# Optimization experiments

Hardware: AMD Instinct MI355X
Metric: run time of the kernel (lower is better)

The kernel has to match this reference:

```python
import jax, jax.numpy as jnp
import numpy as np

N0 = 1373      # hardcoded node-type split in the original forward
TAO = 0.4
EPS = 1e-12


def _l2norm(x, axis):
    # matches torch F.normalize(p=2): x / max(||x||, eps)
    n = jnp.sqrt(jnp.sum(x * x, axis=axis, keepdims=True))
    return x / jnp.maximum(n, EPS)


def setup_inputs() -> dict:
    key = jax.random.key(0)
    ks = jax.random.split(key, 12)
    N, E, D_IN, F, H, D = 20000, 320000, 256, 32, 8, 32
    feat = jax.random.normal(ks[0], (N, D_IN), jnp.float32)
    sloc = jax.random.normal(ks[1], (N, D), jnp.float32)
    topo_fea = jax.random.normal(ks[2], (N, D), jnp.float32)
    src = jax.random.randint(ks[3], (E,), 0, N)
    dst = jax.random.randint(ks[4], (E,), 0, N)
    e_feat = jax.random.randint(ks[5], (E,), 0, 4)
    s = 1.0 / np.sqrt(D_IN)
    W_proj0 = jax.random.normal(ks[6], (D_IN, H * F), jnp.float32) * s
    W_proj1 = jax.random.normal(ks[7], (D_IN, H * F), jnp.float32) * s
    W_prob = jax.random.normal(ks[8], (H, F, F), jnp.float32) * (1.0 / np.sqrt(F))
    W_res0 = jax.random.normal(ks[9], (D_IN, H * F), jnp.float32) * s
    W_res1 = jax.random.normal(ks[10], (D_IN, H * F), jnp.float32) * s
    etype_attn = jnp.ones((4,), jnp.float32)
    return dict(feat=feat, sloc=sloc, topo_fea=topo_fea, src=src, dst=dst,
                e_feat=e_feat, W_proj0=W_proj0, W_proj1=W_proj1, W_prob=W_prob,
                W_res0=W_res0, W_res1=W_res1, etype_attn=etype_attn)


def reference(feat, sloc, topo_fea, src, dst, e_feat,
              W_proj0, W_proj1, W_prob, W_res0, W_res1, etype_attn):
    N = feat.shape[0]
    H, F = W_prob.shape[0], W_prob.shape[2]
    sloc3 = sloc[:, None, :]        # (N,1,D) -- .unsqueeze(1)
    topo3 = topo_fea[:, None, :]

    # per-type node projection
    feat_src = jnp.concatenate(
        [feat[:N0] @ W_proj0, feat[N0:] @ W_proj1], axis=0).reshape(N, H, F)
    # per-head attention feature: softmax(tanh(fc4prob_i(.)), dim=feat)
    ft_attn = jax.nn.softmax(
        jnp.tanh(jnp.einsum('nhf,hfg->nhg', feat_src, W_prob)), axis=2)
    # F.normalize over the NODE dimension (dim=0), as in original
    ft_norm = _l2norm(feat_src, axis=0)

    sloc_n = _l2norm(sloc3, axis=2)
    topo_n = _l2norm(topo3, axis=2)

    # edge attention scores
    a = jnp.sum(ft_attn[dst] * ft_norm[src], axis=2, keepdims=True)   # (E,H,1)
    cos_s = jnp.sum(sloc_n[src] * sloc_n[dst], axis=2, keepdims=True)  # (E,1,1)
    cos_t = jnp.sum(topo_n[src] * topo_n[dst], axis=2, keepdims=True)
    sim = (TAO * cos_s + (1.0 - TAO) * cos_t + 1.0) / 2.0             # (E,1,1)
    e = (sim * a * etype_attn[e_feat][:, None, None])[:, :, 0]        # (E,H)

    # edge softmax: segment softmax over incoming edges of each dst node
    m = jax.ops.segment_max(e, dst, num_segments=N)                   # (N,H)
    ex = jnp.exp(e - m[dst])
    z = jax.ops.segment_sum(ex, dst, num_segments=N)
    att = ex / z[dst]                                                 # (E,H)

    # three u_mul_e + sum aggregations
    aw = att[:, :, None]                                              # (E,H,1)
    rst = jax.ops.segment_sum(feat_src[src] * aw, dst, num_segments=N)  # (N,H,F)
    sl2 = jax.ops.segment_sum(sloc3[src] * aw, dst, num_segments=N)     # (N,H,D)
    tp2 = jax.ops.segment_sum(topo3[src] * aw, dst, num_segments=N)     # (N,H,D)

    resval = jnp.concatenate(
        [feat[:N0] @ W_res0, feat[N0:] @ W_res1], axis=0).reshape(N, H, F)
    out_fea = jax.nn.relu(rst + resval).mean(axis=1)   # (N,F)
    out_sloc = (sl2 + sloc3).mean(axis=1)              # (N,D)
    out_topo = (tp2 + topo3).mean(axis=1)              # (N,D)
    return out_fea, out_sloc, out_topo
```

## Files before the change

kernel.cpp:

```cpp
#include <hip/hip_runtime.h>
#include <math.h>

#define HN0 1373
#define BM 128
#define BN 128
#define BK 32
#define LDT 40

typedef __attribute__((ext_vector_type(8))) short short8;
typedef __attribute__((ext_vector_type(4))) float f32x4;

__device__ inline unsigned short f2bf(float f) {
  unsigned int u = __float_as_uint(f);
  unsigned int r = (u + 0x7FFFu + ((u >> 16) & 1u)) >> 16;
  return (unsigned short)r;
}
__device__ inline float bflo(unsigned int u) { return __uint_as_float(u << 16); }
__device__ inline float bfhi(unsigned int u) { return __uint_as_float(u & 0xFFFF0000u); }

__device__ inline uint4 pack8bf(float4 a, float4 b) {
  uint4 o;
  o.x = (unsigned)f2bf(a.x) | ((unsigned)f2bf(a.y) << 16);
  o.y = (unsigned)f2bf(a.z) | ((unsigned)f2bf(a.w) << 16);
  o.z = (unsigned)f2bf(b.x) | ((unsigned)f2bf(b.y) << 16);
  o.w = (unsigned)f2bf(b.z) | ((unsigned)f2bf(b.w) << 16);
  return o;
}

__global__ __launch_bounds__(256) void prep(
    const float* __restrict__ Wp0, const float* __restrict__ Wr0,
    const float* __restrict__ Wp1, const float* __restrict__ Wr1,
    unsigned short* __restrict__ BTw,
    const float* __restrict__ sloc, const float* __restrict__ topo,
    float* __restrict__ inv_s, float* __restrict__ inv_t,
    unsigned short* __restrict__ slt,
    const int* __restrict__ dst, int* __restrict__ deg, int N, int E) {
  int b = blockIdx.x;
  int tid = threadIdx.x;
  int nodeBlocks = (N + 7) / 8;
  if (b < 1024) {
    int n = b & 511, g = b >> 9;
    const float* W;
    if (g == 0) W = (n < 256) ? Wp0 : Wr0;
    else        W = (n < 256) ? Wp1 : Wr1;
    int c = n & 255;
    BTw[(size_t)g * 512 * 256 + (size_t)n * 256 + tid] = f2bf(W[(size_t)tid * 256 + c]);
  } else if (b < 1024 + nodeBlocks) {
    int node = (b - 1024) * 8 + (tid >> 5);
    int d = tid & 31;
    if (node >= N) return;
    float s = sloc[(size_t)node * 32 + d];
    float t = topo[(size_t)node * 32 + d];
    float ss = s * s, tt = t * t;
#pragma unroll
    for (int m = 16; m >= 1; m >>= 1) {
      ss += __shfl_xor(ss, m);
      tt += __shfl_xor(tt, m);
    }
    if (d == 0) {
      inv_s[node] = 1.f / fmaxf(sqrtf(ss), 1e-12f);
      inv_t[node] = 1.f / fmaxf(sqrtf(tt), 1e-12f);
    }
    slt[(size_t)node * 64 + d] = f2bf(s);
    slt[(size_t)node * 64 + 32 + d] = f2bf(t);
  } else {
    int e = (b - 1024 - nodeBlocks) * 256 + tid;
    if (e < E) atomicAdd(&deg[dst[e]], 1);
  }
}

__global__ __launch_bounds__(256) void gemm_mfma(
    const float* __restrict__ A, const unsigned short* __restrict__ BTw,
    unsigned short* __restrict__ feat_bf, float* __restrict__ resval, int N) {
  __shared__ __align__(16) unsigned short As[BM * LDT];
  __shared__ __align__(16) unsigned short Bs[BN * LDT];
  int tid = threadIdx.x;
  int lane = tid & 63;
  int w = tid >> 6;
  int wr = w >> 1, wc = w & 1;

  int g0t = (HN0 + BM - 1) / BM;
  int bx = blockIdx.x;
  bool g1 = bx >= g0t;
  int rowBase = g1 ? HN0 + (bx - g0t) * BM : bx * BM;
  int rowEnd = g1 ? N : HN0;
  const unsigned short* BT = BTw + (g1 ? (size_t)512 * 256 : 0);
  int colBase = blockIdx.y * BN;

  int r0 = tid >> 2;
  int kp = (tid & 3) << 3;
  int ar1 = min(rowBase + r0, rowEnd - 1);
  int ar2 = min(rowBase + r0 + 64, rowEnd - 1);
  const float* aP1 = A + (size_t)ar1 * 256 + kp;
  const float* aP2 = A + (size_t)ar2 * 256 + kp;
  const unsigned short* bP1 = BT + (size_t)(colBase + r0) * 256 + kp;
  const unsigned short* bP2 = bP1 + (size_t)64 * 256;
  int wo1 = r0 * LDT + kp;
  int wo2 = (r0 + 64) * LDT + kp;

  int q = lane >> 4;
  int fr = lane & 15;
  int aOff = (wr * 64 + fr) * LDT + q * 8;
  int bOff = (wc * 64 + fr) * LDT + q * 8;

  f32x4 acc[4][4] = {};

  float4 fa1a = *reinterpret_cast<const float4*>(aP1);
  float4 fa1b = *reinterpret_cast<const float4*>(aP1 + 4);
  float4 fa2a = *reinterpret_cast<const float4*>(aP2);
  float4 fa2b = *reinterpret_cast<const float4*>(aP2 + 4);
  uint4 rb1 = *reinterpret_cast<const uint4*>(bP1);
  uint4 rb2 = *reinterpret_cast<const uint4*>(bP2);

  for (int t = 0; t < 8; ++t) {
    *reinterpret_cast<uint4*>(&As[wo1]) = pack8bf(fa1a, fa1b);
    *reinterpret_cast<uint4*>(&As[wo2]) = pack8bf(fa2a, fa2b);
    *reinterpret_cast<uint4*>(&Bs[wo1]) = rb1;
    *reinterpret_cast<uint4*>(&Bs[wo2]) = rb2;
    __syncthreads();
    if (t < 7) {
      int ko = (t + 1) * BK;
      fa1a = *reinterpret_cast<const float4*>(aP1 + ko);
      fa1b = *reinterpret_cast<const float4*>(aP1 + ko + 4);
      fa2a = *reinterpret_cast<const float4*>(aP2 + ko);
      fa2b = *reinterpret_cast<const float4*>(aP2 + ko + 4);
      rb1 = *reinterpret_cast<const uint4*>(bP1 + ko);
      rb2 = *reinterpret_cast<const uint4*>(bP2 + ko);
    }
    short8 af[4], bf4[4];
#pragma unroll
    for (int i = 0; i < 4; ++i) {
      af[i] = *reinterpret_cast<const short8*>(&As[aOff + i * 16 * LDT]);
      bf4[i] = *reinterpret_cast<const short8*>(&Bs[bOff + i * 16 * LDT]);
    }
#pragma unroll
    for (int i = 0; i < 4; ++i)
#pragma unroll
      for (int j = 0; j < 4; ++j)
        acc[i][j] = __builtin_amdgcn_mfma_f32_16x16x32_bf16(af[i], bf4[j], acc[i][j], 0, 0, 0);
    __syncthreads();
  }

  if (colBase < 256) {
#pragma unroll
    for (int i = 0; i < 4; ++i) {
      int rb = rowBase + wr * 64 + i * 16 + q * 4;
#pragma unroll
      for (int j = 0; j < 4; ++j) {
        int col = colBase + wc * 64 + j * 16 + fr;
        f32x4 v = acc[i][j];
#pragma unroll
        for (int rr = 0; rr < 4; ++rr) {
          int r = rb + rr;
          if (r < rowEnd) feat_bf[(size_t)r * 256 + col] = f2bf(v[rr]);
        }
      }
    }
  } else {
    int cOff = colBase - 256;
#pragma unroll
    for (int i = 0; i < 4; ++i) {
      int rb = rowBase + wr * 64 + i * 16 + q * 4;
#pragma unroll
      for (int j = 0; j < 4; ++j) {
        int col = cOff + wc * 64 + j * 16 + fr;
        f32x4 v = acc[i][j];
#pragma unroll
        for (int rr = 0; rr < 4; ++rr) {
          int r = rb + rr;
          if (r < rowEnd) resval[(size_t)r * 256 + col] = v[rr];
        }
      }
    }
  }
}

__global__ __launch_bounds__(256) void attn_probs(
    const unsigned short* __restrict__ feat_bf, const float* __restrict__ W_prob,
    unsigned short* __restrict__ ft_attn, float* __restrict__ col_ss, int N) {
  __shared__ float WL[8192];
  __shared__ float fsL[16 * 256];
  int tid = threadIdx.x;
  for (int i = tid; i < 8192; i += 256) WL[i] = W_prob[i];
  int nodeBase = blockIdx.x * 16;
  float ssp = 0.f;
  for (int i = 0; i < 16; ++i) {
    int n = nodeBase + i;
    float v = (n < N) ? __uint_as_float((unsigned)feat_bf[(size_t)n * 256 + tid] << 16) : 0.f;
    fsL[i * 256 + tid] = v;
    ssp += v * v;
  }
  atomicAdd(&col_ss[tid], ssp);
  __syncthreads();
  int h = tid >> 5, g = tid & 31;
  for (int i = 0; i < 16; ++i) {
    int n = nodeBase + i;
    if (n >= N) break;
    float t = 0.f;
    const float* wp = &WL[h * 1024 + g];
    const float* fr = &fsL[i * 256 + h * 32];
#pragma unroll
    for (int f = 0; f < 32; ++f) t = fmaf(fr[f], wp[f * 32], t);
    t = tanhf(t);
    float mx = t;
#pragma unroll
    for (int s = 16; s >= 1; s >>= 1) mx = fmaxf(mx, __shfl_xor(mx, s));
    float ex = __expf(t - mx);
    float sm = ex;
#pragma unroll
    for (int s = 16; s >= 1; s >>= 1) sm += __shfl_xor(sm, s);
    ft_attn[(size_t)n * 256 + tid] = f2bf(ex / sm);
  }
}

__global__ __launch_bounds__(512) void scan_block(const int* __restrict__ deg,
                                                  int* __restrict__ start,
                                                  int* __restrict__ bsum, int n) {
  __shared__ int buf[512];
  int tid = threadIdx.x;
  int gid = blockIdx.x * 512 + tid;
  int v = (gid < n) ? deg[gid] : 0;
  buf[tid] = v;
  __syncthreads();
  for (int off = 1; off < 512; off <<= 1) {
    int t = (tid >= off) ? buf[tid - off] : 0;
    __syncthreads();
    buf[tid] += t;
    __syncthreads();
  }
  if (gid < n) start[gid] = buf[tid] - v;
  if (tid == 511) bsum[blockIdx.x] = buf[511];
}

__global__ __launch_bounds__(256) void mid_small(float* __restrict__ col_ss,
                                                 int* __restrict__ bsum, int nb) {
  int tid = threadIdx.x;
  col_ss[tid] = 1.f / fmaxf(sqrtf(col_ss[tid]), 1e-12f);
  __shared__ int buf[128];
  if (tid < nb) buf[tid] = bsum[tid];
  __syncthreads();
  if (tid == 0) {
    int run = 0;
    for (int i = 0; i < nb; ++i) { int v = buf[i]; buf[i] = run; run += v; }
  }
  __syncthreads();
  if (tid < nb) bsum[tid] = buf[tid];
}

__global__ __launch_bounds__(256) void fill_sim(
    const int* __restrict__ src, const int* __restrict__ dst,
    const int* __restrict__ e_feat, const float* __restrict__ etype_attn,
    const unsigned short* __restrict__ slt,
    const float* __restrict__ inv_s, const float* __restrict__ inv_t,
    const int* __restrict__ start, const int* __restrict__ bsum,
    int* __restrict__ cursor, int* __restrict__ csr_src,
    float* __restrict__ csr_w, int E) {
  int tid = threadIdx.x;
  int j = tid & 7;
  int e = blockIdx.x * 32 + (tid >> 3);
  if (e >= E) return;
  int s = src[e], d = dst[e];
  const unsigned short* ps = slt + (size_t)s * 64 + j * 4;
  const unsigned short* pd = slt + (size_t)d * 64 + j * 4;
  uint2 sa = *reinterpret_cast<const uint2*>(ps);
  uint2 sb = *reinterpret_cast<const uint2*>(pd);
  uint2 ta = *reinterpret_cast<const uint2*>(ps + 32);
  uint2 tb = *reinterpret_cast<const uint2*>(pd + 32);
  float cs = bflo(sa.x) * bflo(sb.x) + bfhi(sa.x) * bfhi(sb.x) +
             bflo(sa.y) * bflo(sb.y) + bfhi(sa.y) * bfhi(sb.y);
  float ct = bflo(ta.x) * bflo(tb.x) + bfhi(ta.x) * bfhi(tb.x) +
             bflo(ta.y) * bflo(tb.y) + bfhi(ta.y) * bfhi(tb.y);
#pragma unroll
  for (int m = 4; m >= 1; m >>= 1) {
    cs += __shfl_xor(cs, m);
    ct += __shfl_xor(ct, m);
  }
  if (j == 0) {
    cs *= inv_s[s] * inv_s[d];
    ct *= inv_t[s] * inv_t[d];
    float sim = (0.4f * cs + 0.6f * ct + 1.f) * 0.5f;
    float wv = sim * etype_attn[e_feat[e]];
    int pos = start[d] + bsum[d >> 9] + atomicAdd(&cursor[d], 1);
    csr_src[pos] = s;
    csr_w[pos] = wv;
  }
}

#define GATHER(S, FP, SL, TP)                                                  \
  {                                                                            \
    FP = *reinterpret_cast<const uint2*>(feat_bf + (size_t)(S) * 256 + fb);    \
    const unsigned short* sp_ = slt + (size_t)(S) * 64 + db;                   \
    SL = *reinterpret_cast<const uint2*>(sp_);                                 \
    TP = *reinterpret_cast<const uint2*>(sp_ + 32);                            \
  }

#define CONSUME(FP, SL, TP, WV)                                                \
  {                                                                            \
    float fs0 = bflo(FP.x), fs1 = bfhi(FP.x);                                  \
    float fs2 = bflo(FP.y), fs3 = bfhi(FP.y);                                  \
    float pa = ai4.x * fs0 + ai4.y * fs1 + ai4.z * fs2 + ai4.w * fs3;          \
    pa += __shfl_xor(pa, 1);                                                   \
    pa += __shfl_xor(pa, 2);                                                   \
    pa += __shfl_xor(pa, 4);                                                   \
    float p = __expf(pa * WV);                                                 \
    l += p;                                                                    \
    accf.x = fmaf(p, fs0, accf.x); accf.y = fmaf(p, fs1, accf.y);              \
    accf.z = fmaf(p, fs2, accf.z); accf.w = fmaf(p, fs3, accf.w);              \
    accs.x = fmaf(p, bflo(SL.x), accs.x); accs.y = fmaf(p, bfhi(SL.x), accs.y);\
    accs.z = fmaf(p, bflo(SL.y), accs.z); accs.w = fmaf(p, bfhi(SL.y), accs.w);\
    acct.x = fmaf(p, bflo(TP.x), acct.x); acct.y = fmaf(p, bfhi(TP.x), acct.y);\
    acct.z = fmaf(p, bflo(TP.y), acct.z); acct.w = fmaf(p, bfhi(TP.y), acct.w);\
  }

__global__ __launch_bounds__(256) void edge_aggregate(
    const unsigned short* __restrict__ feat_bf, const float* __restrict__ resval,
    const unsigned short* __restrict__ ft_attn, const float* __restrict__ inv_cn,
    const unsigned short* __restrict__ slt,
    const float* __restrict__ sloc, const float* __restrict__ topo,
    const int* __restrict__ start, const int* __restrict__ bsum,
    const int* __restrict__ deg,
    const int* __restrict__ csr_src, const float* __restrict__ csr_w,
    float* __restrict__ out, int N) {
  int wave = threadIdx.x >> 6;
  int n = blockIdx.x * 4 + wave;
  if (n >= N) return;
  int lane = threadIdx.x & 63;
  int j = lane & 7;
  int fb = (lane >> 3) * 32 + j * 4;
  int db = j * 4;

  uint2 at2 = *reinterpret_cast<const uint2*>(ft_attn + (size_t)n * 256 + fb);
  float4 icn4 = *reinterpret_cast<const float4*>(inv_cn + fb);
  float4 ai4 = make_float4(bflo(at2.x) * icn4.x, bfhi(at2.x) * icn4.y,
                           bflo(at2.y) * icn4.z, bfhi(at2.y) * icn4.w);
  float l = 0.f;
  float4 accf = make_float4(0.f, 0.f, 0.f, 0.f);
  float4 accs = make_float4(0.f, 0.f, 0.f, 0.f);
  float4 acct = make_float4(0.f, 0.f, 0.f, 0.f);
  int s0 = start[n] + bsum[n >> 9];
  int dg = deg[n];

  int sA = 0, sB = 0;
  float wA = 0.f, wB = 0.f;
  uint2 fpA, slA, tpA, fpB, slB, tpB;
  fpA = fpB = slA = slB = tpA = tpB = make_uint2(0u, 0u);
  if (dg > 0) {
    sA = csr_src[s0]; wA = csr_w[s0];
    GATHER(sA, fpA, slA, tpA);
  }
  if (dg > 1) {
    sB = csr_src[s0 + 1]; wB = csr_w[s0 + 1];
    GATHER(sB, fpB, slB, tpB);
  }
  int i = 0;
  for (; i + 1 < dg; i += 2) {
    CONSUME(fpA, slA, tpA, wA);
    if (i + 2 < dg) {
      sA = csr_src[s0 + i + 2]; wA = csr_w[s0 + i + 2];
      GATHER(sA, fpA, slA, tpA);
    }
    CONSUME(fpB, slB, tpB, wB);
    if (i + 3 < dg) {
      sB = csr_src[s0 + i + 3]; wB = csr_w[s0 + i + 3];
      GATHER(sB, fpB, slB, tpB);
    }
  }
  if (i < dg) CONSUME(fpA, slA, tpA, wA);

  float invl = (l > 0.f) ? 1.f / l : 0.f;

  float4 res4 = *reinterpret_cast<const float4*>(resval + (size_t)n * 256 + fb);
  float4 of = make_float4(fmaxf(fmaf(accf.x, invl, res4.x), 0.f),
                          fmaxf(fmaf(accf.y, invl, res4.y), 0.f),
                          fmaxf(fmaf(accf.z, invl, res4.z), 0.f),
                          fmaxf(fmaf(accf.w, invl, res4.w), 0.f));
  float4 os = make_float4(accs.x * invl, accs.y * invl, accs.z * invl, accs.w * invl);
  float4 ot = make_float4(acct.x * invl, acct.y * invl, acct.z * invl, acct.w * invl);
#pragma unroll
  for (int msk = 8; msk <= 32; msk <<= 1) {
    of.x += __shfl_xor(of.x, msk); of.y += __shfl_xor(of.y, msk);
    of.z += __shfl_xor(of.z, msk); of.w += __shfl_xor(of.w, msk);
    os.x += __shfl_xor(os.x, msk); os.y += __shfl_xor(os.y, msk);
    os.z += __shfl_xor(os.z, msk); os.w += __shfl_xor(os.w, msk);
    ot.x += __shfl_xor(ot.x, msk); ot.y += __shfl_xor(ot.y, msk);
    ot.z += __shfl_xor(ot.z, msk); ot.w += __shfl_xor(ot.w, msk);
  }
  if (lane < 8) {
    float4 sln = *reinterpret_cast<const float4*>(sloc + (size_t)n * 32 + db);
    float4 tpn = *reinterpret_cast<const float4*>(topo + (size_t)n * 32 + db);
    float4 o0 = make_float4(of.x * 0.125f, of.y * 0.125f, of.z * 0.125f, of.w * 0.125f);
    float4 o1 = make_float4(fmaf(os.x, 0.125f, sln.x), fmaf(os.y, 0.125f, sln.y),
                            fmaf(os.z, 0.125f, sln.z), fmaf(os.w, 0.125f, sln.w));
    float4 o2 = make_float4(fmaf(ot.x, 0.125f, tpn.x), fmaf(ot.y, 0.125f, tpn.y),
                            fmaf(ot.z, 0.125f, tpn.z), fmaf(ot.w, 0.125f, tpn.w));
    *reinterpret_cast<float4*>(out + (size_t)n * 32 + db) = o0;
    *reinterpret_cast<float4*>(out + (size_t)N * 32 + (size_t)n * 32 + db) = o1;
    *reinterpret_cast<float4*>(out + (size_t)2 * N * 32 + (size_t)n * 32 + db) = o2;
  }
}

extern "C" void kernel_launch(void* const* d_in, const int* in_sizes, int n_in,
                              void* d_out, int out_size, void* d_ws, size_t ws_size,
                              hipStream_t stream) {
  const float* feat = (const float*)d_in[0];
  const float* sloc = (const float*)d_in[1];
  const float* topo = (const float*)d_in[2];
  const int* src = (const int*)d_in[3];
  const int* dst = (const int*)d_in[4];
  const int* e_feat = (const int*)d_in[5];
  const float* W_proj0 = (const float*)d_in[6];
  const float* W_proj1 = (const float*)d_in[7];
  const float* W_prob = (const float*)d_in[8];
  const float* W_res0 = (const float*)d_in[9];
  const float* W_res1 = (const float*)d_in[10];
  const float* etype_attn = (const float*)d_in[11];
  int E = in_sizes[3];
  int N = in_sizes[1] / 32;
  float* out = (float*)d_out;

  char* ws = (char*)d_ws;
  size_t off = 0;
  auto alloc = [&](size_t bytes) -> char* {
    char* p = ws + off;
    off += (bytes + 255) & ~(size_t)255;
    return p;
  };
  int* deg = (int*)alloc((size_t)N * 4);
  int* cursor = (int*)alloc((size_t)N * 4);
  float* col_ss = (float*)alloc(256 * 4);
  size_t zeroBytes = ((char*)col_ss + 256 * 4) - (char*)deg;
  int* startArr = (int*)alloc(((size_t)N + 1) * 4);
  int* bsum = (int*)alloc(128 * 4);
  float* inv_s = (float*)alloc((size_t)N * 4);
  float* inv_t = (float*)alloc((size_t)N * 4);
  int* csr_src = (int*)alloc((size_t)E * 4);
  float* csr_w = (float*)alloc((size_t)E * 4);
  unsigned short* feat_bf = (unsigned short*)alloc((size_t)N * 256 * 2);
  unsigned short* slt = (unsigned short*)alloc((size_t)N * 64 * 2);
  float* resval = (float*)alloc((size_t)N * 256 * 4);
  unsigned short* ft_attn = (unsigned short*)alloc((size_t)N * 256 * 2);
  unsigned short* BTw = (unsigned short*)alloc((size_t)2 * 512 * 256 * 2);

  hipMemsetAsync(deg, 0, zeroBytes, stream);

  int nodeBlocks = (N + 7) / 8;
  int degBlocks = (E + 255) / 256;
  prep<<<1024 + nodeBlocks + degBlocks, 256, 0, stream>>>(
      W_proj0, W_res0, W_proj1, W_res1, BTw, sloc, topo, inv_s, inv_t, slt,
      dst, deg, N, E);

  int g0t = (HN0 + BM - 1) / BM;
  int g1t = (N - HN0 + BM - 1) / BM;
  gemm_mfma<<<dim3(g0t + g1t, 4), 256, 0, stream>>>(feat, BTw, feat_bf, resval, N);

  attn_probs<<<(N + 15) / 16, 256, 0, stream>>>(feat_bf, W_prob, ft_attn, col_ss, N);

  int nb = (N + 511) / 512;
  scan_block<<<nb, 512, 0, stream>>>(deg, startArr, bsum, N);
  mid_small<<<1, 256, 0, stream>>>(col_ss, bsum, nb);

  fill_sim<<<(E + 31) / 32, 256, 0, stream>>>(src, dst, e_feat, etype_attn, slt,
                                              inv_s, inv_t, startArr, bsum,
                                              cursor, csr_src, csr_w, E);

  edge_aggregate<<<(N + 3) / 4, 256, 0, stream>>>(feat_bf, resval, ft_attn, col_ss,
                                                  slt, sloc, topo, startArr, bsum, deg,
                                                  csr_src, csr_w, out, N);
}
```

Baseline: 191.0 us.

## Store resval in bf16, pack CSR as int2, deepen gather pipeline, shrink blocks

The residual GEMM output is now stored as bf16 instead of fp32, which halves its write and read traffic. The CSR source index and weight are interleaved into a single int2 array so each edge needs one load. The edge_aggregate prefetch is raised from two to three edges in flight, and the kernel runs 128-thread blocks with two nodes per block instead of four. The bf16 residual adds rounding error to the feature output.

```diff
diff --git a/kernel.cpp b/kernel.cpp
--- a/kernel.cpp
+++ b/kernel.cpp
@@ -71,7 +71,8 @@
 
 __global__ __launch_bounds__(256) void gemm_mfma(
     const float* __restrict__ A, const unsigned short* __restrict__ BTw,
-    unsigned short* __restrict__ feat_bf, float* __restrict__ resval, int N) {
+    unsigned short* __restrict__ feat_bf, unsigned short* __restrict__ resval,
+    int N) {
   __shared__ __align__(16) unsigned short As[BM * LDT];
   __shared__ __align__(16) unsigned short Bs[BN * LDT];
   int tid = threadIdx.x;
@@ -141,35 +142,19 @@
     __syncthreads();
   }
 
-  if (colBase < 256) {
-#pragma unroll
-    for (int i = 0; i < 4; ++i) {
-      int rb = rowBase + wr * 64 + i * 16 + q * 4;
-#pragma unroll
-      for (int j = 0; j < 4; ++j) {
-        int col = colBase + wc * 64 + j * 16 + fr;
-        f32x4 v = acc[i][j];
-#pragma unroll
-        for (int rr = 0; rr < 4; ++rr) {
-          int r = rb + rr;
-          if (r < rowEnd) feat_bf[(size_t)r * 256 + col] = f2bf(v[rr]);
-        }
-      }
-    }
-  } else {
-    int cOff = colBase - 256;
-#pragma unroll
-    for (int i = 0; i < 4; ++i) {
-      int rb = rowBase + wr * 64 + i * 16 + q * 4;
-#pragma unroll
-      for (int j = 0; j < 4; ++j) {
-        int col = cOff + wc * 64 + j * 16 + fr;
-        f32x4 v = acc[i][j];
-#pragma unroll
-        for (int rr = 0; rr < 4; ++rr) {
-          int r = rb + rr;
-          if (r < rowEnd) resval[(size_t)r * 256 + col] = v[rr];
-        }
+  unsigned short* outp = (colBase < 256) ? feat_bf : resval;
+  int cOff = colBase & 255;
+#pragma unroll
+  for (int i = 0; i < 4; ++i) {
+    int rb = rowBase + wr * 64 + i * 16 + q * 4;
+#pragma unroll
+    for (int j = 0; j < 4; ++j) {
+      int col = cOff + wc * 64 + j * 16 + fr;
+      f32x4 v = acc[i][j];
+#pragma unroll
+      for (int rr = 0; rr < 4; ++rr) {
+        int r = rb + rr;
+        if (r < rowEnd) outp[(size_t)r * 256 + col] = f2bf(v[rr]);
       }
     }
   }
@@ -253,8 +238,7 @@
     const unsigned short* __restrict__ slt,
     const float* __restrict__ inv_s, const float* __restrict__ inv_t,
     const int* __restrict__ start, const int* __restrict__ bsum,
-    int* __restrict__ cursor, int* __restrict__ csr_src,
-    float* __restrict__ csr_w, int E) {
+    int* __restrict__ cursor, int2* __restrict__ csr, int E) {
   int tid = threadIdx.x;
   int j = tid & 7;
   int e = blockIdx.x * 32 + (tid >> 3);
@@ -281,28 +265,34 @@
     float sim = (0.4f * cs + 0.6f * ct + 1.f) * 0.5f;
     float wv = sim * etype_attn[e_feat[e]];
     int pos = start[d] + bsum[d >> 9] + atomicAdd(&cursor[d], 1);
-    csr_src[pos] = s;
-    csr_w[pos] = wv;
-  }
-}
-
-#define GATHER(S, FP, SL, TP)                                                  \
-  {                                                                            \
-    FP = *reinterpret_cast<const uint2*>(feat_bf + (size_t)(S) * 256 + fb);    \
-    const unsigned short* sp_ = slt + (size_t)(S) * 64 + db;                   \
+    csr[pos] = make_int2(s, __float_as_int(wv));
+  }
+}
+
+#define LOADIDX(K, V, W)                                                       \
+  do {                                                                         \
+    int2 c_ = csr[s0 + (K)];                                                   \
+    V = c_.x;                                                                  \
+    W = __int_as_float(c_.y);                                                  \
+  } while (0)
+
+#define GATHER(V, FP, SL, TP)                                                  \
+  do {                                                                         \
+    FP = *reinterpret_cast<const uint2*>(feat_bf + (size_t)(V) * 256 + fb);    \
+    const unsigned short* sp_ = slt + (size_t)(V) * 64 + db;                   \
     SL = *reinterpret_cast<const uint2*>(sp_);                                 \
     TP = *reinterpret_cast<const uint2*>(sp_ + 32);                            \
-  }
-
-#define CONSUME(FP, SL, TP, WV)                                                \
-  {                                                                            \
+  } while (0)
+
+#define CONSUME(W, FP, SL, TP)                                                 \
+  do {                                                                         \
     float fs0 = bflo(FP.x), fs1 = bfhi(FP.x);                                  \
     float fs2 = bflo(FP.y), fs3 = bfhi(FP.y);                                  \
     float pa = ai4.x * fs0 + ai4.y * fs1 + ai4.z * fs2 + ai4.w * fs3;          \
     pa += __shfl_xor(pa, 1);                                                   \
     pa += __shfl_xor(pa, 2);                                                   \
     pa += __shfl_xor(pa, 4);                                                   \
-    float p = __expf(pa * WV);                                                 \
+    float p = __expf(pa * (W));                                                \
     l += p;                                                                    \
     accf.x = fmaf(p, fs0, accf.x); accf.y = fmaf(p, fs1, accf.y);              \
     accf.z = fmaf(p, fs2, accf.z); accf.w = fmaf(p, fs3, accf.w);              \
@@ -310,19 +300,18 @@
     accs.z = fmaf(p, bflo(SL.y), accs.z); accs.w = fmaf(p, bfhi(SL.y), accs.w);\
     acct.x = fmaf(p, bflo(TP.x), acct.x); acct.y = fmaf(p, bfhi(TP.x), acct.y);\
     acct.z = fmaf(p, bflo(TP.y), acct.z); acct.w = fmaf(p, bfhi(TP.y), acct.w);\
-  }
-
-__global__ __launch_bounds__(256) void edge_aggregate(
-    const unsigned short* __restrict__ feat_bf, const float* __restrict__ resval,
+  } while (0)
+
+__global__ __launch_bounds__(128) void edge_aggregate(
+    const unsigned short* __restrict__ feat_bf, const unsigned short* __restrict__ resval,
     const unsigned short* __restrict__ ft_attn, const float* __restrict__ inv_cn,
     const unsigned short* __restrict__ slt,
     const float* __restrict__ sloc, const float* __restrict__ topo,
     const int* __restrict__ start, const int* __restrict__ bsum,
-    const int* __restrict__ deg,
-    const int* __restrict__ csr_src, const float* __restrict__ csr_w,
+    const int* __restrict__ deg, const int2* __restrict__ csr,
     float* __restrict__ out, int N) {
   int wave = threadIdx.x >> 6;
-  int n = blockIdx.x * 4 + wave;
+  int n = blockIdx.x * 2 + wave;
   if (n >= N) return;
   int lane = threadIdx.x & 63;
   int j = lane & 7;
@@ -340,40 +329,33 @@
   int s0 = start[n] + bsum[n >> 9];
   int dg = deg[n];
 
-  int sA = 0, sB = 0;
-  float wA = 0.f, wB = 0.f;
-  uint2 fpA, slA, tpA, fpB, slB, tpB;
-  fpA = fpB = slA = slB = tpA = tpB = make_uint2(0u, 0u);
-  if (dg > 0) {
-    sA = csr_src[s0]; wA = csr_w[s0];
-    GATHER(sA, fpA, slA, tpA);
-  }
-  if (dg > 1) {
-    sB = csr_src[s0 + 1]; wB = csr_w[s0 + 1];
-    GATHER(sB, fpB, slB, tpB);
-  }
+  int vA = 0, vB = 0, vC = 0;
+  float wA = 0.f, wB = 0.f, wC = 0.f;
+  uint2 fpA = make_uint2(0u, 0u), fpB = make_uint2(0u, 0u), fpC = make_uint2(0u, 0u);
+  uint2 slA = make_uint2(0u, 0u), slB = make_uint2(0u, 0u), slC = make_uint2(0u, 0u);
+  uint2 tpA = make_uint2(0u, 0u), tpB = make_uint2(0u, 0u), tpC = make_uint2(0u, 0u);
+  if (dg > 0) { LOADIDX(0, vA, wA); GATHER(vA, fpA, slA, tpA); }
+  if (dg > 1) { LOADIDX(1, vB, wB); GATHER(vB, fpB, slB, tpB); }
+  if (dg > 2) { LOADIDX(2, vC, wC); GATHER(vC, fpC, slC, tpC); }
   int i = 0;
-  for (; i + 1 < dg; i += 2) {
-    CONSUME(fpA, slA, tpA, wA);
-    if (i + 2 < dg) {
-      sA = csr_src[s0 + i + 2]; wA = csr_w[s0 + i + 2];
-      GATHER(sA, fpA, slA, tpA);
-    }
-    CONSUME(fpB, slB, tpB, wB);
-    if (i + 3 < dg) {
-      sB = csr_src[s0 + i + 3]; wB = csr_w[s0 + i + 3];
-      GATHER(sB, fpB, slB, tpB);
-    }
-  }
-  if (i < dg) CONSUME(fpA, slA, tpA, wA);
+  for (; i + 2 < dg; i += 3) {
+    CONSUME(wA, fpA, slA, tpA);
+    if (i + 3 < dg) { LOADIDX(i + 3, vA, wA); GATHER(vA, fpA, slA, tpA); }
+    CONSUME(wB, fpB, slB, tpB);
+    if (i + 4 < dg) { LOADIDX(i + 4, vB, wB); GATHER(vB, fpB, slB, tpB); }
+    CONSUME(wC, fpC, slC, tpC);
+    if (i + 5 < dg) { LOADIDX(i + 5, vC, wC); GATHER(vC, fpC, slC, tpC); }
+  }
+  if (i < dg) CONSUME(wA, fpA, slA, tpA);
+  if (i + 1 < dg) CONSUME(wB, fpB, slB, tpB);
 
   float invl = (l > 0.f) ? 1.f / l : 0.f;
 
-  float4 res4 = *reinterpret_cast<const float4*>(resval + (size_t)n * 256 + fb);
-  float4 of = make_float4(fmaxf(fmaf(accf.x, invl, res4.x), 0.f),
-                          fmaxf(fmaf(accf.y, invl, res4.y), 0.f),
-                          fmaxf(fmaf(accf.z, invl, res4.z), 0.f),
-                          fmaxf(fmaf(accf.w, invl, res4.w), 0.f));
+  uint2 res2 = *reinterpret_cast<const uint2*>(resval + (size_t)n * 256 + fb);
+  float4 of = make_float4(fmaxf(fmaf(accf.x, invl, bflo(res2.x)), 0.f),
+                          fmaxf(fmaf(accf.y, invl, bfhi(res2.x)), 0.f),
+                          fmaxf(fmaf(accf.z, invl, bflo(res2.y)), 0.f),
+                          fmaxf(fmaf(accf.w, invl, bfhi(res2.y)), 0.f));
   float4 os = make_float4(accs.x * invl, accs.y * invl, accs.z * invl, accs.w * invl);
   float4 ot = make_float4(acct.x * invl, acct.y * invl, acct.z * invl, acct.w * invl);
 #pragma unroll
@@ -433,11 +415,10 @@
   int* bsum = (int*)alloc(128 * 4);
   float* inv_s = (float*)alloc((size_t)N * 4);
   float* inv_t = (float*)alloc((size_t)N * 4);
-  int* csr_src = (int*)alloc((size_t)E * 4);
-  float* csr_w = (float*)alloc((size_t)E * 4);
+  int2* csr = (int2*)alloc((size_t)E * 8);
   unsigned short* feat_bf = (unsigned short*)alloc((size_t)N * 256 * 2);
   unsigned short* slt = (unsigned short*)alloc((size_t)N * 64 * 2);
-  float* resval = (float*)alloc((size_t)N * 256 * 4);
+  unsigned short* resval = (unsigned short*)alloc((size_t)N * 256 * 2);
   unsigned short* ft_attn = (unsigned short*)alloc((size_t)N * 256 * 2);
   unsigned short* BTw = (unsigned short*)alloc((size_t)2 * 512 * 256 * 2);
 
@@ -461,9 +442,9 @@
 
   fill_sim<<<(E + 31) / 32, 256, 0, stream>>>(src, dst, e_feat, etype_attn, slt,
                                               inv_s, inv_t, startArr, bsum,
-                                              cursor, csr_src, csr_w, E);
-
-  edge_aggregate<<<(N + 3) / 4, 256, 0, stream>>>(feat_bf, resval, ft_attn, col_ss,
-                                                  slt, sloc, topo, startArr, bsum, deg,
-                                                  csr_src, csr_w, out, N);
-}
+                                              cursor, csr, E);
+
+  edge_aggregate<<<(N + 1) / 2, 128, 0, stream>>>(feat_bf, resval, ft_attn, col_ss,
+                                                  slt, sloc, topo, startArr, bsum,
+                                                  deg, csr, out, N);
+}
```

After: 190.2 us. About the same (-0.4%).
